# Kernel optimization log

Hardware: AMD Instinct MI355X
Metric: run time of the kernel (lower is better)

Reference implementation:

```python
import jax, jax.numpy as jnp
import numpy as np

B, S, D = 2, 2048, 1024
H, KVH, HD = 16, 1, 64
E, K, HID = 8, 2, 4096
EPS = 1e-5


def rmsnorm(x, scale):
    ms = jnp.mean(x * x, axis=-1, keepdims=True)
    return x * jax.lax.rsqrt(ms + EPS) * scale


def setup_inputs() -> dict:
    key = jax.random.key(0)
    ks = jax.random.split(key, 12)
    s = lambda k, shape, fan: jax.random.normal(k, shape, jnp.float32) * (fan ** -0.5)
    return {
        "x": jax.random.normal(ks[0], (B, S, D), jnp.float32),
        "g_pre_mqa": jnp.ones((D,), jnp.float32),
        "g_post_mqa": jnp.ones((D,), jnp.float32),
        "g_pre_moe": jnp.ones((D,), jnp.float32),
        "g_post_moe": jnp.ones((D,), jnp.float32),
        "Wq": s(ks[1], (D, H * HD), D),
        "Wk": s(ks[2], (D, KVH * HD), D),
        "Wv": s(ks[3], (D, KVH * HD), D),
        "Wo": s(ks[4], (H * HD, D), H * HD),
        "Wg": s(ks[5], (D, E), D),
        "We1": s(ks[6], (E, D, HID), D),
        "We2": s(ks[7], (E, HID, D), HID),
    }


def mqa(x, Wq, Wk, Wv, Wo):
    b, s, _ = x.shape
    q = (x @ Wq).reshape(b, s, H, HD).transpose(0, 2, 1, 3)     # [B,H,S,hd]
    k = (x @ Wk).reshape(b, s, KVH, HD).transpose(0, 2, 1, 3)   # [B,1,S,hd]
    v = (x @ Wv).reshape(b, s, KVH, HD).transpose(0, 2, 1, 3)
    scores = jnp.einsum('bhqd,bhkd->bhqk', q, jnp.broadcast_to(k, (b, H, s, HD))) / np.sqrt(HD)
    probs = jax.nn.softmax(scores, axis=-1)  # note: no causal mask, matching _standard_attention
    out = jnp.einsum('bhqk,bhkd->bhqd', probs, jnp.broadcast_to(v, (b, H, s, HD)))
    out = out.transpose(0, 2, 1, 3).reshape(b, s, H * HD)
    return out @ Wo


def moe(h, Wg, We1, We2):
    logits = h @ Wg                       # [B,S,E]
    probs = jax.nn.softmax(logits, axis=-1)
    topv, topi = jax.lax.top_k(probs, K)  # [B,S,K]
    # scatter top-k probs into full expert vector (non-chosen experts -> 0)
    routing = jnp.sum(jax.nn.one_hot(topi, E, dtype=h.dtype) * topv[..., None], axis=-2)  # [B,S,E]
    mid = jax.nn.gelu(jnp.einsum('bsd,edh->bseh', h, We1))
    eo = jnp.einsum('bseh,ehd->bsed', mid, We2)
    out = jnp.einsum('bse,bsed->bsd', routing, eo)
    return out, probs


def reference(x, g_pre_mqa, g_post_mqa, g_pre_moe, g_post_moe, Wq, Wk, Wv, Wo, Wg, We1, We2):
    # inference path: dropout and router noise disabled (training=False)
    x = x + rmsnorm(mqa(rmsnorm(x, g_pre_mqa), Wq, Wk, Wv, Wo), g_post_mqa)
    moe_out, routing_probs = moe(rmsnorm(x, g_pre_moe), Wg, We1, We2)
    x = x + rmsnorm(moe_out, g_post_moe)
    return x, routing_probs
```

## Files before the change

kernel.cpp:

```cpp
#include <hip/hip_runtime.h>
#include <hip/hip_bf16.h>
#include <math.h>

#define NTOK   4096
#define DMODEL 1024
#define SEQL   2048
#define QKVW   1152
#define NH     16
#define HDIM   64
#define NE     8
#define HIDD   4096
#define EPSV   1e-5f
#define KT     32

#define ASCL   256.f
#define WSCL   4096.f
#define OUTSCL (1.f/1048576.f)
#define SSCALE (0.125f/65536.f)
#define PBIAS  10.397207708399179f
#define DTHR   0.5f

typedef __attribute__((ext_vector_type(8))) short bf16x8;
typedef __attribute__((ext_vector_type(8))) _Float16 f16x8;
typedef __attribute__((ext_vector_type(4))) _Float16 f16x4;
typedef __attribute__((ext_vector_type(4))) float f32x4;

#define GLOBAL_AS __attribute__((address_space(1)))
#define LDS_AS    __attribute__((address_space(3)))
__device__ __forceinline__ void gl_lds16(const void* g, void* l){
  __builtin_amdgcn_global_load_lds((const GLOBAL_AS void*)g, (LDS_AS void*)l, 16u, 0, 0u);
}

__device__ __forceinline__ short f2b(float x){
  __hip_bfloat16 h = __float2bfloat16(x);
  return *reinterpret_cast<short*>(&h);
}
__device__ __forceinline__ void split2h(float x, _Float16& a, _Float16& b){
  a = (_Float16)x;
  b = (_Float16)(x - (float)a);
}

__global__ __launch_bounds__(256) void transpose_conv_kernel(
    const float* __restrict__ in, short* __restrict__ out,
    int R, int C, long inb, long outb)
{
  __shared__ float tile[32][33];
  in  += (size_t)blockIdx.z * inb;
  out += (size_t)blockIdx.z * outb;
  int c0 = blockIdx.x*32, r0 = blockIdx.y*32;
  int tx = threadIdx.x & 31, ty = threadIdx.x >> 5;
  #pragma unroll
  for (int i=0;i<4;i++)
    tile[ty+i*8][tx] = in[(size_t)(r0+ty+i*8)*C + c0+tx];
  __syncthreads();
  int cl = threadIdx.x >> 3, quad = threadIdx.x & 7;
  short4 s;
  s.x = f2b(tile[quad*4+0][cl]);
  s.y = f2b(tile[quad*4+1][cl]);
  s.z = f2b(tile[quad*4+2][cl]);
  s.w = f2b(tile[quad*4+3][cl]);
  *(short4*)&out[(size_t)(c0+cl)*R + r0 + quad*4] = s;
}

__global__ __launch_bounds__(256) void transpose_split2f16_kernel(
    const float* __restrict__ in, _Float16* __restrict__ o1, _Float16* __restrict__ o2,
    int R, int C, int rowOff, int outLD)
{
  __shared__ float tile[32][33];
  int c0 = blockIdx.x*32, r0 = blockIdx.y*32;
  int tx = threadIdx.x & 31, ty = threadIdx.x >> 5;
  #pragma unroll
  for (int i=0;i<4;i++)
    tile[ty+i*8][tx] = in[(size_t)(r0+ty+i*8)*C + c0+tx];
  __syncthreads();
  #pragma unroll
  for (int i=0;i<4;i++){
    float v = tile[tx][ty+i*8] * WSCL;
    _Float16 va,vb; split2h(v,va,vb);
    size_t idx = (size_t)(c0+ty+i*8+rowOff)*outLD + r0+tx;
    o1[idx]=va; o2[idx]=vb;
  }
}

__global__ __launch_bounds__(256) void rms_split2_kernel(
    const float* __restrict__ x, const float* __restrict__ g,
    _Float16* __restrict__ o1, _Float16* __restrict__ o2)
{
  int row = blockIdx.x, tid = threadIdx.x;
  const float4* xr = (const float4*)(x + (size_t)row*DMODEL);
  float4 v = xr[tid];
  float ss = v.x*v.x + v.y*v.y + v.z*v.z + v.w*v.w;
  #pragma unroll
  for (int off=32; off; off>>=1) ss += __shfl_down(ss, off);
  __shared__ float red[4];
  if ((tid&63)==0) red[tid>>6] = ss;
  __syncthreads();
  float rs = rsqrtf((red[0]+red[1]+red[2]+red[3])*(1.f/1024.f) + EPSV) * ASCL;
  float4 gv = ((const float4*)g)[tid];
  float o[4] = {v.x*rs*gv.x, v.y*rs*gv.y, v.z*rs*gv.z, v.w*rs*gv.w};
  f16x4 s1,s2;
  #pragma unroll
  for (int c=0;c<4;c++){ _Float16 a,b; split2h(o[c],a,b); s1[c]=a; s2[c]=b; }
  size_t base = (size_t)row*DMODEL + tid*4;
  *(f16x4*)(o1+base) = s1; *(f16x4*)(o2+base) = s2;
}

__global__ __launch_bounds__(256) void vtrans_split2_kernel(
    const _Float16* __restrict__ p1, const _Float16* __restrict__ p2,
    _Float16* __restrict__ o1, _Float16* __restrict__ o2)
{
  __shared__ float tile[32][33];
  int s0 = blockIdx.x*32, d0 = blockIdx.y*32, bb = blockIdx.z;
  int tx = threadIdx.x & 31, ty = threadIdx.x >> 5;
  #pragma unroll
  for (int i=0;i<4;i++){
    size_t idx = (size_t)(bb*SEQL + s0+ty+i*8)*QKVW + DMODEL+HDIM + d0+tx;
    tile[ty+i*8][tx] = (float)p1[idx] + (float)p2[idx];
  }
  __syncthreads();
  #pragma unroll
  for (int i=0;i<4;i++){
    float v = tile[tx][ty+i*8];
    _Float16 va,vb; split2h(v,va,vb);
    size_t idx = (size_t)(bb*HDIM + d0+ty+i*8)*SEQL + s0+tx;
    o1[idx]=va; o2[idx]=vb;
  }
}

__global__ __launch_bounds__(256) void gemm_f16x2_kernel(
    const _Float16* __restrict__ a1, const _Float16* __restrict__ a2,
    const _Float16* __restrict__ b1, const _Float16* __restrict__ b2,
    float* __restrict__ C, int K, int ldc, float outscale)
{
  __shared__ _Float16 lsA[2][128*32];
  __shared__ _Float16 lsB[2][128*32];
  int m0 = blockIdx.y*128, n0 = blockIdx.x*128;
  int tid = threadIdx.x, wave = tid>>6, lane = tid&63;
  int g = lane>>4, li = lane&15;
  int wm = (wave>>1)*64, wn = (wave&1)*64;
  const _Float16* Ap[2] = {a1,a2};
  const _Float16* Bp[2] = {b1,b2};
  int srow = wave*32 + (lane>>2), scol = (lane&3)*8;
  const _Float16* gA[2][2]; const _Float16* gB[2][2];
  #pragma unroll
  for (int p=0;p<2;p++)
    #pragma unroll
    for (int i=0;i<2;i++){
      gA[p][i] = Ap[p] + (size_t)(m0+srow+i*16)*K + scol;
      gB[p][i] = Bp[p] + (size_t)(n0+srow+i*16)*K + scol;
    }
  f32x4 acc[4][4] = {};
  for (int k0=0; k0<K; k0+=32){
    #pragma unroll
    for (int p=0;p<2;p++)
      #pragma unroll
      for (int i=0;i<2;i++){
        gl_lds16(gA[p][i]+k0, &lsA[p][(wave*32+i*16)*32]);
        gl_lds16(gB[p][i]+k0, &lsB[p][(wave*32+i*16)*32]);
      }
    __syncthreads();
    #pragma unroll
    for (int i=0;i<2;i++){
      f16x8 af[4];
      #pragma unroll
      for (int m=0;m<4;m++) af[m] = *(f16x8*)&lsA[i][(wm+m*16+li)*32 + g*8];
      #pragma unroll
      for (int j=0;j<2-i;j++){
        #pragma unroll
        for (int n=0;n<4;n++){
          f16x8 bfr = *(f16x8*)&lsB[j][(wn+n*16+li)*32 + g*8];
          #pragma unroll
          for (int m=0;m<4;m++)
            acc[m][n] = __builtin_amdgcn_mfma_f32_16x16x32_f16(af[m], bfr, acc[m][n], 0,0,0);
        }
      }
    }
    __syncthreads();
  }
  #pragma unroll
  for (int m=0;m<4;m++){
    int lr0 = wm + m*16 + g*4;
    #pragma unroll
    for (int n=0;n<4;n++){
      int col = n0 + wn + n*16 + li;
      #pragma unroll
      for (int r=0;r<4;r++)
        C[(size_t)(m0+lr0+r)*ldc + col] = acc[m][n][r]*outscale;
    }
  }
}

__global__ __launch_bounds__(256) void gemm_f16x2s_kernel(
    const _Float16* __restrict__ a1, const _Float16* __restrict__ a2,
    const _Float16* __restrict__ b1, const _Float16* __restrict__ b2,
    _Float16* __restrict__ o1, _Float16* __restrict__ o2, int K, int ldc, float outscale)
{
  __shared__ _Float16 lsA[2][128*32];
  __shared__ _Float16 lsB[2][128*32];
  int m0 = blockIdx.y*128, n0 = blockIdx.x*128;
  int tid = threadIdx.x, wave = tid>>6, lane = tid&63;
  int g = lane>>4, li = lane&15;
  int wm = (wave>>1)*64, wn = (wave&1)*64;
  const _Float16* Ap[2] = {a1,a2};
  const _Float16* Bp[2] = {b1,b2};
  int srow = wave*32 + (lane>>2), scol = (lane&3)*8;
  const _Float16* gA[2][2]; const _Float16* gB[2][2];
  #pragma unroll
  for (int p=0;p<2;p++)
    #pragma unroll
    for (int i=0;i<2;i++){
      gA[p][i] = Ap[p] + (size_t)(m0+srow+i*16)*K + scol;
      gB[p][i] = Bp[p] + (size_t)(n0+srow+i*16)*K + scol;
    }
  f32x4 acc[4][4] = {};
  for (int k0=0; k0<K; k0+=32){
    #pragma unroll
    for (int p=0;p<2;p++)
      #pragma unroll
      for (int i=0;i<2;i++){
        gl_lds16(gA[p][i]+k0, &lsA[p][(wave*32+i*16)*32]);
        gl_lds16(gB[p][i]+k0, &lsB[p][(wave*32+i*16)*32]);
      }
    __syncthreads();
    #pragma unroll
    for (int i=0;i<2;i++){
      f16x8 af[4];
      #pragma unroll
      for (int m=0;m<4;m++) af[m] = *(f16x8*)&lsA[i][(wm+m*16+li)*32 + g*8];
      #pragma unroll
      for (int j=0;j<2-i;j++){
        #pragma unroll
        for (int n=0;n<4;n++){
          f16x8 bfr = *(f16x8*)&lsB[j][(wn+n*16+li)*32 + g*8];
          #pragma unroll
          for (int m=0;m<4;m++)
            acc[m][n] = __builtin_amdgcn_mfma_f32_16x16x32_f16(af[m], bfr, acc[m][n], 0,0,0);
        }
      }
    }
    __syncthreads();
  }
  #pragma unroll
  for (int m=0;m<4;m++){
    int lr0 = wm + m*16 + g*4;
    #pragma unroll
    for (int n=0;n<4;n++){
      int col = n0 + wn + n*16 + li;
      #pragma unroll
      for (int r=0;r<4;r++){
        float val = acc[m][n][r]*outscale;
        _Float16 xa,xb; split2h(val,xa,xb);
        size_t idx = (size_t)(m0+lr0+r)*ldc + col;
        o1[idx]=xa; o2[idx]=xb;
      }
    }
  }
}

__global__ __launch_bounds__(256) void attn_f16_kernel(
    const _Float16* __restrict__ q1, const _Float16* __restrict__ q2,
    const _Float16* __restrict__ v1, const _Float16* __restrict__ v2,
    _Float16* __restrict__ o1, _Float16* __restrict__ o2)
{
  __shared__ _Float16 Ks[32*136];
  __shared__ _Float16 Vs[64*72];
  int qt = blockIdx.x, h = blockIdx.y, b = blockIdx.z;
  int tid = threadIdx.x, wave = tid>>6, lane = tid&63;
  int g = lane>>4, li = lane&15;
  size_t qbase = (size_t)b*SEQL + qt*128;
  const _Float16* qsrc[2] = {q1,q2};
  const _Float16* vsrc[2] = {v1,v2};
  f16x8 qf[2][2][2];
  #pragma unroll
  for (int nf=0;nf<2;nf++){
    size_t qrow = qbase + wave*32 + nf*16 + li;
    #pragma unroll
    for (int j=0;j<2;j++)
      #pragma unroll
      for (int kk=0;kk<2;kk++)
        qf[nf][j][kk] = *(const f16x8*)(qsrc[j] + qrow*QKVW + h*HDIM + kk*32 + g*8);
  }
  const _Float16* kga[2]; int klds[2];
  const _Float16* vga[2]; int vlds[2];
  #pragma unroll
  for (int i=0;i<2;i++){
    int c = tid + 256*i;
    { int row=c>>4, sub=c&15, pl=sub>>3, d=(sub&7)*8;
      kga[i] = qsrc[pl] + ((size_t)b*SEQL + row)*QKVW + DMODEL + d;
      klds[i] = row*136 + pl*64 + d; }
    { int row=c>>3, sub=c&7, pl=sub>>2, s8=(sub&3)*8;
      vga[i] = vsrc[pl] + ((size_t)b*HDIM + row)*SEQL + s8;
      vlds[i] = row*72 + pl*32 + s8; }
  }
  f16x8 kreg[2], vreg[2];
  #pragma unroll
  for (int i=0;i<2;i++){ kreg[i]=*(const f16x8*)kga[i]; vreg[i]=*(const f16x8*)vga[i]; }

  float m_run[2] = {-1e30f,-1e30f}, l_run[2] = {0.f,0.f};
  f32x4 acc_o[4][2] = {};
  int src1 = (((2*g)&3)<<4) + li;
  int src2 = (((2*g+1)&3)<<4) + li;
  bool hi_half = (g>=2);

  for (int kvt=0; kvt<SEQL/KT; kvt++){
    #pragma unroll
    for (int i=0;i<2;i++){
      *(f16x8*)&Ks[klds[i]] = kreg[i];
      *(f16x8*)&Vs[vlds[i]] = vreg[i];
    }
    __syncthreads();
    if (kvt+1 < SEQL/KT){
      #pragma unroll
      for (int i=0;i<2;i++){
        kreg[i] = *(const f16x8*)(kga[i] + (size_t)(kvt+1)*KT*QKVW);
        vreg[i] = *(const f16x8*)(vga[i] + (size_t)(kvt+1)*KT);
      }
    }
    f32x4 s_acc[2][2] = {};
    __builtin_amdgcn_s_setprio(1);
    #pragma unroll
    for (int i=0;i<2;i++){
      #pragma unroll
      for (int kk=0;kk<2;kk++){
        f16x8 af[2];
        #pragma unroll
        for (int mf=0;mf<2;mf++)
          af[mf] = *(f16x8*)&Ks[(mf*16+li)*136 + i*64 + kk*32 + g*8];
        #pragma unroll
        for (int j=0;j<2-i;j++){
          #pragma unroll
          for (int nf=0;nf<2;nf++){
            #pragma unroll
            for (int mf=0;mf<2;mf++)
              s_acc[mf][nf] = __builtin_amdgcn_mfma_f32_16x16x32_f16(af[mf], qf[nf][j][kk], s_acc[mf][nf], 0,0,0);
          }
        }
      }
    }
    __builtin_amdgcn_s_setprio(0);
    float p[2][2][4];
    #pragma unroll
    for (int nf=0;nf<2;nf++){
      float mx = -1e30f;
      #pragma unroll
      for (int mf=0;mf<2;mf++)
        #pragma unroll
        for (int r=0;r<4;r++) mx = fmaxf(mx, s_acc[mf][nf][r]);
      mx = fmaxf(mx, __shfl_xor(mx,16));
      mx = fmaxf(mx, __shfl_xor(mx,32));
      mx *= SSCALE;
      if (!__all(mx <= m_run[nf] + DTHR)){
        float mn = fmaxf(m_run[nf], mx);
        float al = __expf(m_run[nf] - mn);
        m_run[nf] = mn;
        l_run[nf] *= al;
        #pragma unroll
        for (int mfd=0; mfd<4; mfd++){
          acc_o[mfd][nf][0]*=al; acc_o[mfd][nf][1]*=al;
          acc_o[mfd][nf][2]*=al; acc_o[mfd][nf][3]*=al;
        }
      }
      float rsum = 0.f;
      #pragma unroll
      for (int mf=0;mf<2;mf++)
        #pragma unroll
        for (int r=0;r<4;r++){
          float pv = __expf(s_acc[mf][nf][r]*SSCALE - m_run[nf] + PBIAS);
          p[mf][nf][r] = pv; rsum += pv;
        }
      rsum += __shfl_xor(rsum,16);
      rsum += __shfl_xor(rsum,32);
      l_run[nf] += rsum;
    }
    f16x8 fp_frag[2][2];
    #pragma unroll
    for (int nf=0;nf<2;nf++){
      float p8[8];
      #pragma unroll
      for (int jj=0;jj<4;jj++){
        float v0 = __shfl(p[0][nf][jj], src1);
        float vv1 = __shfl(p[1][nf][jj], src1);
        p8[jj] = hi_half ? vv1 : v0;
        float w0 = __shfl(p[0][nf][jj], src2);
        float w1 = __shfl(p[1][nf][jj], src2);
        p8[4+jj] = hi_half ? w1 : w0;
      }
      #pragma unroll
      for (int jj=0;jj<8;jj++){
        _Float16 xa,xb; split2h(p8[jj], xa,xb);
        fp_frag[nf][0][jj]=xa; fp_frag[nf][1][jj]=xb;
      }
    }
    __builtin_amdgcn_s_setprio(1);
    #pragma unroll
    for (int vj=0;vj<2;vj++){
      f16x8 av[4];
      #pragma unroll
      for (int mfd=0;mfd<4;mfd++)
        av[mfd] = *(f16x8*)&Vs[(mfd*16+li)*72 + vj*32 + g*8];
      #pragma unroll
      for (int pi=0; pi<2-vj; pi++)
        #pragma unroll
        for (int mfd=0;mfd<4;mfd++)
          #pragma unroll
          for (int nf=0;nf<2;nf++)
            acc_o[mfd][nf] = __builtin_amdgcn_mfma_f32_16x16x32_f16(av[mfd], fp_frag[nf][pi], acc_o[mfd][nf], 0,0,0);
    }
    __builtin_amdgcn_s_setprio(0);
    __syncthreads();
  }
  #pragma unroll
  for (int nf=0;nf<2;nf++){
    float inv = 1.f/l_run[nf];
    size_t q = qbase + wave*32 + nf*16 + li;
    #pragma unroll
    for (int mfd=0;mfd<4;mfd++){
      int d0 = mfd*16 + g*4;
      f16x4 sa,sb;
      #pragma unroll
      for (int r=0;r<4;r++){
        _Float16 xa,xb; split2h(acc_o[mfd][nf][r]*inv, xa,xb);
        sa[r]=xa; sb[r]=xb;
      }
      size_t base = q*DMODEL + h*HDIM + d0;
      *(f16x4*)(o1+base)=sa; *(f16x4*)(o2+base)=sb;
    }
  }
}

__global__ __launch_bounds__(256) void attnres_kernel(
    const float* __restrict__ x, const float* __restrict__ ao,
    const float* __restrict__ gpost, const float* __restrict__ gpre,
    float* __restrict__ x2, short* __restrict__ h)
{
  int row = blockIdx.x, tid = threadIdx.x;
  float4 a  = ((const float4*)(ao + (size_t)row*DMODEL))[tid];
  float4 xv = ((const float4*)(x  + (size_t)row*DMODEL))[tid];
  float ss = a.x*a.x + a.y*a.y + a.z*a.z + a.w*a.w;
  #pragma unroll
  for (int off=32; off; off>>=1) ss += __shfl_down(ss, off);
  __shared__ float red[4];
  if ((tid&63)==0) red[tid>>6] = ss;
  __syncthreads();
  float rs1 = rsqrtf((red[0]+red[1]+red[2]+red[3])*(1.f/1024.f) + EPSV);
  float4 gp = ((const float4*)gpost)[tid];
  float4 o;
  o.x = xv.x + a.x*rs1*gp.x; o.y = xv.y + a.y*rs1*gp.y;
  o.z = xv.z + a.z*rs1*gp.z; o.w = xv.w + a.w*rs1*gp.w;
  ((float4*)(x2 + (size_t)row*DMODEL))[tid] = o;
  float s2 = o.x*o.x + o.y*o.y + o.z*o.z + o.w*o.w;
  __syncthreads();
  #pragma unroll
  for (int off=32; off; off>>=1) s2 += __shfl_down(s2, off);
  if ((tid&63)==0) red[tid>>6] = s2;
  __syncthreads();
  float rs2 = rsqrtf((red[0]+red[1]+red[2]+red[3])*(1.f/1024.f) + EPSV);
  float4 gm = ((const float4*)gpre)[tid];
  short4 hs;
  hs.x = f2b(o.x*rs2*gm.x); hs.y = f2b(o.y*rs2*gm.y);
  hs.z = f2b(o.z*rs2*gm.z); hs.w = f2b(o.w*rs2*gm.w);
  *(short4*)(h + (size_t)row*DMODEL + tid*4) = hs;
}

__global__ __launch_bounds__(64) void router_kernel(
    const float* __restrict__ x2, const float* __restrict__ g, const float* __restrict__ Wg,
    float* __restrict__ probs_out, int* __restrict__ tok_list, float* __restrict__ w_list,
    int* __restrict__ counts)
{
  int t = blockIdx.x, lane = threadIdx.x;
  const float4* xr = (const float4*)(x2 + (size_t)t*DMODEL);
  float4 v[4]; float ss = 0.f;
  #pragma unroll
  for (int i=0;i<4;i++){ v[i] = xr[lane + 64*i];
    ss += v[i].x*v[i].x + v[i].y*v[i].y + v[i].z*v[i].z + v[i].w*v[i].w; }
  #pragma unroll
  for (int off=32; off; off>>=1) ss += __shfl_xor(ss, off);
  float rs = rsqrtf(ss*(1.f/1024.f) + EPSV);
  float le[8] = {0,0,0,0,0,0,0,0};
  #pragma unroll
  for (int i=0;i<4;i++){
    int jb = (lane + 64*i)*4;
    float hv[4] = {v[i].x, v[i].y, v[i].z, v[i].w};
    #pragma unroll
    for (int c=0;c<4;c++){
      float hj = hv[c]*rs*g[jb+c];
      const float* wrow = Wg + (size_t)(jb+c)*NE;
      #pragma unroll
      for (int ee=0;ee<8;ee++) le[ee] += hj*wrow[ee];
    }
  }
  #pragma unroll
  for (int ee=0;ee<8;ee++)
    #pragma unroll
    for (int off=32; off; off>>=1) le[ee] += __shfl_xor(le[ee], off);
  float mx = le[0];
  #pragma unroll
  for (int ee=1;ee<8;ee++) mx = fmaxf(mx, le[ee]);
  float p[8], s = 0.f;
  #pragma unroll
  for (int ee=0;ee<8;ee++){ p[ee] = expf(le[ee]-mx); s += p[ee]; }
  float inv = 1.f/s;
  #pragma unroll
  for (int ee=0;ee<8;ee++) p[ee] *= inv;
  if (lane < 8) probs_out[(size_t)t*NE + lane] = p[lane];
  if (lane == 0){
    int i1 = 0;
    #pragma unroll
    for (int ee=1;ee<8;ee++) if (p[ee] > p[i1]) i1 = ee;
    int i2 = (i1==0) ? 1 : 0;
    #pragma unroll
    for (int ee=0;ee<8;ee++) if (ee != i1 && p[ee] > p[i2]) i2 = ee;
    int pos = atomicAdd(&counts[i1], 1);
    tok_list[i1*NTOK+pos] = t;
    w_list[i1*NTOK+pos] = p[i1];
    pos = atomicAdd(&counts[i2], 1);
    tok_list[i2*NTOK+pos] = t | (1<<16);
    w_list[i2*NTOK+pos] = p[i2];
  }
}

__global__ void prefix_kernel(const int* __restrict__ counts, int* __restrict__ bases){
  if (threadIdx.x == 0){
    int a = 0;
    for (int ee=0;ee<8;ee++){ bases[ee] = a; a += counts[ee]; }
  }
}

__global__ __launch_bounds__(256) void moe_gemm1_kernel(
    const short* __restrict__ h, const short* __restrict__ we1t,
    const int* __restrict__ tok_list, const int* __restrict__ counts,
    const int* __restrict__ bases, short* __restrict__ mid)
{
  int e = blockIdx.z;
  int cnt = counts[e];
  int m0 = blockIdx.y*128, n0 = blockIdx.x*128;
  if (m0 >= cnt) return;
  int base = bases[e];
  const short* Bt = we1t + (size_t)e*HIDD*DMODEL;
  const int* tl = tok_list + e*NTOK;
  __shared__ short lsA[128*32];
  __shared__ short lsB[128*32];
  int tid = threadIdx.x, wave = tid>>6, lane = tid&63;
  int li = lane&15, g = lane>>4;
  int wm = (wave>>1)*64, wn = (wave&1)*64;
  int srow = wave*32 + (lane>>2), scol = (lane&3)*8;
  const short* gA[2]; const short* gB[2];
  #pragma unroll
  for (int i=0;i<2;i++){
    int rr = min(m0+srow+i*16, cnt-1);
    gA[i] = h + (size_t)(tl[rr] & 0xFFFF)*DMODEL + scol;
    gB[i] = Bt + (size_t)(n0+srow+i*16)*DMODEL + scol;
  }
  f32x4 acc[4][4] = {};
  for (int k0=0; k0<DMODEL; k0+=32){
    #pragma unroll
    for (int i=0;i<2;i++){
      gl_lds16(gA[i]+k0, &lsA[(wave*32+i*16)*32]);
      gl_lds16(gB[i]+k0, &lsB[(wave*32+i*16)*32]);
    }
    __syncthreads();
    bf16x8 af[4], bfr[4];
    #pragma unroll
    for (int m=0;m<4;m++) af[m] = *(bf16x8*)&lsA[(wm+m*16+li)*32 + g*8];
    #pragma unroll
    for (int n=0;n<4;n++) bfr[n] = *(bf16x8*)&lsB[(wn+n*16+li)*32 + g*8];
    #pragma unroll
    for (int m=0;m<4;m++)
      #pragma unroll
      for (int n=0;n<4;n++)
        acc[m][n] = __builtin_amdgcn_mfma_f32_16x16x32_bf16(af[m], bfr[n], acc[m][n], 0,0,0);
    __syncthreads();
  }
  #pragma unroll
  for (int m=0;m<4;m++){
    int lr0 = wm + m*16 + (g<<2);
    #pragma unroll
    for (int n=0;n<4;n++){
      int col = n0 + wn + n*16 + li;
      #pragma unroll
      for (int r=0;r<4;r++){
        int gr = m0 + lr0 + r;
        if (gr < cnt){
          float tval = acc[m][n][r];
          float u = 1.5957691216057308f*(tval + 0.044715f*tval*tval*tval);
          float ge = tval / (1.f + __expf(-u));
          mid[(size_t)(base+gr)*HIDD + col] = f2b(ge);
        }
      }
    }
  }
}

__global__ __launch_bounds__(256) void moe_gemm2_kernel(
    const short* __restrict__ mid, const short* __restrict__ we2t,
    const int* __restrict__ tok_list, const float* __restrict__ w_list,
    const int* __restrict__ counts, const int* __restrict__ bases,
    float* __restrict__ eo)
{
  int e = blockIdx.z;
  int cnt = counts[e];
  int m0 = blockIdx.y*128, n0 = blockIdx.x*128;
  if (m0 >= cnt) return;
  int base = bases[e];
  const short* A  = mid + (size_t)base*HIDD;
  const short* Bt = we2t + (size_t)e*DMODEL*HIDD;
  const int* tl = tok_list + e*NTOK;
  const float* wl = w_list + e*NTOK;
  __shared__ short lsA[128*32];
  __shared__ short lsB[128*32];
  int tid = threadIdx.x, wave = tid>>6, lane = tid&63;
  int li = lane&15, g = lane>>4;
  int wm = (wave>>1)*64, wn = (wave&1)*64;
  int srow = wave*32 + (lane>>2), scol = (lane&3)*8;
  const short* gA[2]; const short* gB[2];
  #pragma unroll
  for (int i=0;i<2;i++){
    int rr = min(m0+srow+i*16, cnt-1);
    gA[i] = A + (size_t)rr*HIDD + scol;
    gB[i] = Bt + (size_t)(n0+srow+i*16)*HIDD + scol;
  }
  f32x4 acc[4][4] = {};
  for (int k0=0; k0<HIDD; k0+=32){
    #pragma unroll
    for (int i=0;i<2;i++){
      gl_lds16(gA[i]+k0, &lsA[(wave*32+i*16)*32]);
      gl_lds16(gB[i]+k0, &lsB[(wave*32+i*16)*32]);
    }
    __syncthreads();
    bf16x8 af[4], bfr[4];
    #pragma unroll
    for (int m=0;m<4;m++) af[m] = *(bf16x8*)&lsA[(wm+m*16+li)*32 + g*8];
    #pragma unroll
    for (int n=0;n<4;n++) bfr[n] = *(bf16x8*)&lsB[(wn+n*16+li)*32 + g*8];
    #pragma unroll
    for (int m=0;m<4;m++)
      #pragma unroll
      for (int n=0;n<4;n++)
        acc[m][n] = __builtin_amdgcn_mfma_f32_16x16x32_bf16(af[m], bfr[n], acc[m][n], 0,0,0);
    __syncthreads();
  }
  #pragma unroll
  for (int m=0;m<4;m++){
    int lr0 = wm + m*16 + (g<<2);
    #pragma unroll
    for (int n=0;n<4;n++){
      int col = n0 + wn + n*16 + li;
      #pragma unroll
      for (int r=0;r<4;r++){
        int gr = m0 + lr0 + r;
        if (gr < cnt){
          int pv = tl[gr];
          eo[((size_t)(pv>>16)*NTOK + (pv & 0xFFFF))*DMODEL + col] = wl[gr]*acc[m][n][r];
        }
      }
    }
  }
}

__global__ __launch_bounds__(256) void final_kernel(
    const float* __restrict__ x2, const float* __restrict__ eo,
    const float* __restrict__ g, float* __restrict__ out)
{
  int row = blockIdx.x, tid = threadIdx.x;
  float4 m0 = ((const float4*)(eo + (size_t)row*DMODEL))[tid];
  float4 m1 = ((const float4*)(eo + (size_t)(NTOK+row)*DMODEL))[tid];
  float4 mv;
  mv.x = m0.x+m1.x; mv.y = m0.y+m1.y; mv.z = m0.z+m1.z; mv.w = m0.w+m1.w;
  float4 xv = ((const float4*)(x2  + (size_t)row*DMODEL))[tid];
  float ss = mv.x*mv.x + mv.y*mv.y + mv.z*mv.z + mv.w*mv.w;
  #pragma unroll
  for (int off=32; off; off>>=1) ss += __shfl_down(ss, off);
  __shared__ float red[4];
  if ((tid&63)==0) red[tid>>6] = ss;
  __syncthreads();
  float rs = rsqrtf((red[0]+red[1]+red[2]+red[3])*(1.f/1024.f) + EPSV);
  float4 gv = ((const float4*)g)[tid];
  float4 o;
  o.x = xv.x + mv.x*rs*gv.x; o.y = xv.y + mv.y*rs*gv.y;
  o.z = xv.z + mv.z*rs*gv.z; o.w = xv.w + mv.w*rs*gv.w;
  ((float4*)(out + (size_t)row*DMODEL))[tid] = o;
}

extern "C" void kernel_launch(void* const* d_in, const int* in_sizes, int n_in,
                              void* d_out, int out_size, void* d_ws, size_t ws_size,
                              hipStream_t stream) {
  (void)in_sizes; (void)n_in; (void)out_size; (void)ws_size;
  const float* x          = (const float*)d_in[0];
  const float* g_pre_mqa  = (const float*)d_in[1];
  const float* g_post_mqa = (const float*)d_in[2];
  const float* g_pre_moe  = (const float*)d_in[3];
  const float* g_post_moe = (const float*)d_in[4];
  const float* Wq         = (const float*)d_in[5];
  const float* Wk         = (const float*)d_in[6];
  const float* Wv         = (const float*)d_in[7];
  const float* Wo         = (const float*)d_in[8];
  const float* Wg         = (const float*)d_in[9];
  const float* We1        = (const float*)d_in[10];
  const float* We2        = (const float*)d_in[11];

  float* out_x = (float*)d_out;
  float* out_probs = out_x + (size_t)NTOK*DMODEL;

  char* p = (char*)d_ws;
  size_t off = 0;
  auto alloc = [&](size_t bytes)->char*{
    char* r = p + off; off = (off + bytes + 255) & ~(size_t)255; return r; };

  short* we1t = (short*)alloc((size_t)NE*HIDD*DMODEL*2);
  short* we2t = (short*)alloc((size_t)NE*DMODEL*HIDD*2);
  short* mid  = (short*)alloc((size_t)2*NTOK*HIDD*2);

  char* regA = alloc((size_t)2*NTOK*DMODEL*2);
  _Float16* xn1p1 = (_Float16*)regA;
  _Float16* xn1p2 = (_Float16*)(regA + (size_t)NTOK*DMODEL*2);
  float* ao       = (float*)regA;

  _Float16* wqkvT1 = (_Float16*)alloc((size_t)QKVW*DMODEL*2);
  _Float16* wqkvT2 = (_Float16*)alloc((size_t)QKVW*DMODEL*2);
  _Float16* woT1   = (_Float16*)alloc((size_t)DMODEL*DMODEL*2);
  _Float16* woT2   = (_Float16*)alloc((size_t)DMODEL*DMODEL*2);

  char* regB = alloc((size_t)2*NTOK*DMODEL*2);
  _Float16* attnp1 = (_Float16*)regB;
  _Float16* attnp2 = (_Float16*)(regB + (size_t)NTOK*DMODEL*2);

  char* regC = alloc((size_t)2*NTOK*DMODEL*4 + (size_t)NTOK*DMODEL*2);
  _Float16* qkvf1 = (_Float16*)regC;
  _Float16* qkvf2 = (_Float16*)(regC + (size_t)NTOK*QKVW*2);
  float* eo    = (float*)regC;
  short* hbuf  = (short*)(regC + (size_t)2*NTOK*DMODEL*4);

  _Float16* vt1 = (_Float16*)alloc((size_t)2*HDIM*SEQL*2);
  _Float16* vt2 = (_Float16*)alloc((size_t)2*HDIM*SEQL*2);
  float* x2  = (float*)alloc((size_t)NTOK*DMODEL*4);
  int*   tok_l  = (int*)  alloc((size_t)NE*NTOK*4);
  float* w_l    = (float*)alloc((size_t)NE*NTOK*4);
  int*   counts = (int*)  alloc(256);
  int*   bases  = (int*)  alloc(256);

  transpose_conv_kernel<<<dim3(HIDD/32, DMODEL/32, NE), 256, 0, stream>>>(
      We1, we1t, DMODEL, HIDD, (long)DMODEL*HIDD, (long)HIDD*DMODEL);
  transpose_conv_kernel<<<dim3(DMODEL/32, HIDD/32, NE), 256, 0, stream>>>(
      We2, we2t, HIDD, DMODEL, (long)HIDD*DMODEL, (long)DMODEL*HIDD);
  transpose_split2f16_kernel<<<dim3(DMODEL/32, DMODEL/32), 256, 0, stream>>>(
      Wq, wqkvT1, wqkvT2, DMODEL, DMODEL, 0, DMODEL);
  transpose_split2f16_kernel<<<dim3(HDIM/32, DMODEL/32), 256, 0, stream>>>(
      Wk, wqkvT1, wqkvT2, DMODEL, HDIM, DMODEL, DMODEL);
  transpose_split2f16_kernel<<<dim3(HDIM/32, DMODEL/32), 256, 0, stream>>>(
      Wv, wqkvT1, wqkvT2, DMODEL, HDIM, DMODEL+HDIM, DMODEL);
  transpose_split2f16_kernel<<<dim3(DMODEL/32, DMODEL/32), 256, 0, stream>>>(
      Wo, woT1, woT2, DMODEL, DMODEL, 0, DMODEL);

  rms_split2_kernel<<<NTOK, 256, 0, stream>>>(x, g_pre_mqa, xn1p1, xn1p2);
  gemm_f16x2s_kernel<<<dim3(QKVW/128, NTOK/128), 256, 0, stream>>>(
      xn1p1, xn1p2, wqkvT1, wqkvT2, qkvf1, qkvf2, DMODEL, QKVW, OUTSCL*ASCL);
  vtrans_split2_kernel<<<dim3(SEQL/32, HDIM/32, 2), 256, 0, stream>>>(qkvf1, qkvf2, vt1, vt2);
  attn_f16_kernel<<<dim3(SEQL/128, NH, 2), 256, 0, stream>>>(
      qkvf1, qkvf2, vt1, vt2, attnp1, attnp2);
  gemm_f16x2_kernel<<<dim3(DMODEL/128, NTOK/128), 256, 0, stream>>>(
      attnp1, attnp2, woT1, woT2, ao, DMODEL, DMODEL, OUTSCL);
  attnres_kernel<<<NTOK, 256, 0, stream>>>(x, ao, g_post_mqa, g_pre_moe, x2, hbuf);

  hipMemsetAsync(counts, 0, 32, stream);
  router_kernel<<<NTOK, 64, 0, stream>>>(x2, g_pre_moe, Wg, out_probs, tok_l, w_l, counts);
  prefix_kernel<<<1, 64, 0, stream>>>(counts, bases);
  moe_gemm1_kernel<<<dim3(HIDD/128, NTOK/128, NE), 256, 0, stream>>>(
      hbuf, we1t, tok_l, counts, bases, mid);
  moe_gemm2_kernel<<<dim3(DMODEL/128, NTOK/128, NE), 256, 0, stream>>>(
      mid, we2t, tok_l, w_l, counts, bases, eo);
  final_kernel<<<NTOK, 256, 0, stream>>>(x2, eo, g_post_moe, out_x);
}
```

Baseline: 745.5 us.

## Fuse router into attention residual kernel, drop prefix kernel, swap grid axes

Merges the router (gate logits, softmax, top-2 and atomic token-list append) into the post-attention residual/RMSNorm kernel, so x2 is no longer re-read and normalized a second time. The prefix-sum kernel is removed, and each MoE GEMM block now computes its expert base offset from the counts. All GEMM grids swap blockIdx.x and y, so consecutive blocks walk along M rather than N, which changes L2 reuse of weight tiles. The cost is a larger, more serialized tail in the fused kernel (thread 0 does the softmax, top-k and atomics) and a small redundant prefix loop in every GEMM block.

```diff
diff --git a/kernel.cpp b/kernel.cpp
--- a/kernel.cpp
+++ b/kernel.cpp
@@ -134,7 +134,7 @@
 {
   __shared__ _Float16 lsA[2][128*32];
   __shared__ _Float16 lsB[2][128*32];
-  int m0 = blockIdx.y*128, n0 = blockIdx.x*128;
+  int m0 = blockIdx.x*128, n0 = blockIdx.y*128;
   int tid = threadIdx.x, wave = tid>>6, lane = tid&63;
   int g = lane>>4, li = lane&15;
   int wm = (wave>>1)*64, wn = (wave&1)*64;
@@ -197,7 +197,7 @@
 {
   __shared__ _Float16 lsA[2][128*32];
   __shared__ _Float16 lsB[2][128*32];
-  int m0 = blockIdx.y*128, n0 = blockIdx.x*128;
+  int m0 = blockIdx.x*128, n0 = blockIdx.y*128;
   int tid = threadIdx.x, wave = tid>>6, lane = tid&63;
   int g = lane>>4, li = lane&15;
   int wm = (wave>>1)*64, wn = (wave&1)*64;
@@ -428,10 +428,13 @@
   }
 }
 
-__global__ __launch_bounds__(256) void attnres_kernel(
+__global__ __launch_bounds__(256) void attnres_router_kernel(
     const float* __restrict__ x, const float* __restrict__ ao,
     const float* __restrict__ gpost, const float* __restrict__ gpre,
-    float* __restrict__ x2, short* __restrict__ h)
+    const float* __restrict__ Wg,
+    float* __restrict__ x2, short* __restrict__ h,
+    float* __restrict__ probs_out, int* __restrict__ tok_list,
+    float* __restrict__ w_list, int* __restrict__ counts)
 {
   int row = blockIdx.x, tid = threadIdx.x;
   float4 a  = ((const float4*)(ao + (size_t)row*DMODEL))[tid];
@@ -456,86 +459,63 @@
   __syncthreads();
   float rs2 = rsqrtf((red[0]+red[1]+red[2]+red[3])*(1.f/1024.f) + EPSV);
   float4 gm = ((const float4*)gpre)[tid];
+  float n0 = o.x*rs2*gm.x, n1 = o.y*rs2*gm.y, n2 = o.z*rs2*gm.z, n3 = o.w*rs2*gm.w;
   short4 hs;
-  hs.x = f2b(o.x*rs2*gm.x); hs.y = f2b(o.y*rs2*gm.y);
-  hs.z = f2b(o.z*rs2*gm.z); hs.w = f2b(o.w*rs2*gm.w);
+  hs.x = f2b(n0); hs.y = f2b(n1); hs.z = f2b(n2); hs.w = f2b(n3);
   *(short4*)(h + (size_t)row*DMODEL + tid*4) = hs;
-}
-
-__global__ __launch_bounds__(64) void router_kernel(
-    const float* __restrict__ x2, const float* __restrict__ g, const float* __restrict__ Wg,
-    float* __restrict__ probs_out, int* __restrict__ tok_list, float* __restrict__ w_list,
-    int* __restrict__ counts)
-{
-  int t = blockIdx.x, lane = threadIdx.x;
-  const float4* xr = (const float4*)(x2 + (size_t)t*DMODEL);
-  float4 v[4]; float ss = 0.f;
-  #pragma unroll
-  for (int i=0;i<4;i++){ v[i] = xr[lane + 64*i];
-    ss += v[i].x*v[i].x + v[i].y*v[i].y + v[i].z*v[i].z + v[i].w*v[i].w; }
-  #pragma unroll
-  for (int off=32; off; off>>=1) ss += __shfl_xor(ss, off);
-  float rs = rsqrtf(ss*(1.f/1024.f) + EPSV);
-  float le[8] = {0,0,0,0,0,0,0,0};
-  #pragma unroll
-  for (int i=0;i<4;i++){
-    int jb = (lane + 64*i)*4;
-    float hv[4] = {v[i].x, v[i].y, v[i].z, v[i].w};
-    #pragma unroll
-    for (int c=0;c<4;c++){
-      float hj = hv[c]*rs*g[jb+c];
-      const float* wrow = Wg + (size_t)(jb+c)*NE;
-      #pragma unroll
-      for (int ee=0;ee<8;ee++) le[ee] += hj*wrow[ee];
-    }
-  }
-  #pragma unroll
-  for (int ee=0;ee<8;ee++)
-    #pragma unroll
-    for (int off=32; off; off>>=1) le[ee] += __shfl_xor(le[ee], off);
-  float mx = le[0];
-  #pragma unroll
-  for (int ee=1;ee<8;ee++) mx = fmaxf(mx, le[ee]);
-  float p[8], s = 0.f;
-  #pragma unroll
-  for (int ee=0;ee<8;ee++){ p[ee] = expf(le[ee]-mx); s += p[ee]; }
-  float inv = 1.f/s;
-  #pragma unroll
-  for (int ee=0;ee<8;ee++) p[ee] *= inv;
-  if (lane < 8) probs_out[(size_t)t*NE + lane] = p[lane];
-  if (lane == 0){
+  const float* wr = Wg + (size_t)(tid*4)*NE;
+  float le[8];
+  #pragma unroll
+  for (int e=0;e<8;e++)
+    le[e] = n0*wr[e] + n1*wr[NE+e] + n2*wr[2*NE+e] + n3*wr[3*NE+e];
+  #pragma unroll
+  for (int e=0;e<8;e++)
+    #pragma unroll
+    for (int off=32; off; off>>=1) le[e] += __shfl_xor(le[e], off);
+  __shared__ float redl[4][8];
+  if ((tid&63)==0)
+    #pragma unroll
+    for (int e=0;e<8;e++) redl[tid>>6][e] = le[e];
+  __syncthreads();
+  if (tid == 0){
+    float l[8];
+    #pragma unroll
+    for (int e=0;e<8;e++) l[e] = redl[0][e]+redl[1][e]+redl[2][e]+redl[3][e];
+    float mx = l[0];
+    #pragma unroll
+    for (int e=1;e<8;e++) mx = fmaxf(mx, l[e]);
+    float pp[8], s = 0.f;
+    #pragma unroll
+    for (int e=0;e<8;e++){ pp[e] = expf(l[e]-mx); s += pp[e]; }
+    float inv = 1.f/s;
+    #pragma unroll
+    for (int e=0;e<8;e++){ pp[e] *= inv; probs_out[(size_t)row*NE + e] = pp[e]; }
     int i1 = 0;
     #pragma unroll
-    for (int ee=1;ee<8;ee++) if (p[ee] > p[i1]) i1 = ee;
+    for (int e=1;e<8;e++) if (pp[e] > pp[i1]) i1 = e;
     int i2 = (i1==0) ? 1 : 0;
     #pragma unroll
-    for (int ee=0;ee<8;ee++) if (ee != i1 && p[ee] > p[i2]) i2 = ee;
+    for (int e=0;e<8;e++) if (e != i1 && pp[e] > pp[i2]) i2 = e;
     int pos = atomicAdd(&counts[i1], 1);
-    tok_list[i1*NTOK+pos] = t;
-    w_list[i1*NTOK+pos] = p[i1];
+    tok_list[i1*NTOK+pos] = row;
+    w_list[i1*NTOK+pos] = pp[i1];
     pos = atomicAdd(&counts[i2], 1);
-    tok_list[i2*NTOK+pos] = t | (1<<16);
-    w_list[i2*NTOK+pos] = p[i2];
-  }
-}
-
-__global__ void prefix_kernel(const int* __restrict__ counts, int* __restrict__ bases){
-  if (threadIdx.x == 0){
-    int a = 0;
-    for (int ee=0;ee<8;ee++){ bases[ee] = a; a += counts[ee]; }
+    tok_list[i2*NTOK+pos] = row | (1<<16);
+    w_list[i2*NTOK+pos] = pp[i2];
   }
 }
 
 __global__ __launch_bounds__(256) void moe_gemm1_kernel(
     const short* __restrict__ h, const short* __restrict__ we1t,
     const int* __restrict__ tok_list, const int* __restrict__ counts,
-    const int* __restrict__ bases, short* __restrict__ mid)
+    short* __restrict__ mid)
 {
   int e = blockIdx.z;
   int cnt = counts[e];
-  int m0 = blockIdx.y*128, n0 = blockIdx.x*128;
+  int m0 = blockIdx.x*128, n0 = blockIdx.y*128;
   if (m0 >= cnt) return;
-  int base = bases[e];
+  int base = 0;
+  for (int j=0;j<NE;j++){ int c = counts[j]; if (j<e) base += c; }
   const short* Bt = we1t + (size_t)e*HIDD*DMODEL;
   const int* tl = tok_list + e*NTOK;
   __shared__ short lsA[128*32];
@@ -594,14 +574,14 @@
 __global__ __launch_bounds__(256) void moe_gemm2_kernel(
     const short* __restrict__ mid, const short* __restrict__ we2t,
     const int* __restrict__ tok_list, const float* __restrict__ w_list,
-    const int* __restrict__ counts, const int* __restrict__ bases,
-    float* __restrict__ eo)
+    const int* __restrict__ counts, float* __restrict__ eo)
 {
   int e = blockIdx.z;
   int cnt = counts[e];
-  int m0 = blockIdx.y*128, n0 = blockIdx.x*128;
+  int m0 = blockIdx.x*128, n0 = blockIdx.y*128;
   if (m0 >= cnt) return;
-  int base = bases[e];
+  int base = 0;
+  for (int j=0;j<NE;j++){ int c = counts[j]; if (j<e) base += c; }
   const short* A  = mid + (size_t)base*HIDD;
   const short* Bt = we2t + (size_t)e*DMODEL*HIDD;
   const int* tl = tok_list + e*NTOK;
@@ -736,7 +716,6 @@
   int*   tok_l  = (int*)  alloc((size_t)NE*NTOK*4);
   float* w_l    = (float*)alloc((size_t)NE*NTOK*4);
   int*   counts = (int*)  alloc(256);
-  int*   bases  = (int*)  alloc(256);
 
   transpose_conv_kernel<<<dim3(HIDD/32, DMODEL/32, NE), 256, 0, stream>>>(
       We1, we1t, DMODEL, HIDD, (long)DMODEL*HIDD, (long)HIDD*DMODEL);
@@ -752,21 +731,20 @@
       Wo, woT1, woT2, DMODEL, DMODEL, 0, DMODEL);
 
   rms_split2_kernel<<<NTOK, 256, 0, stream>>>(x, g_pre_mqa, xn1p1, xn1p2);
-  gemm_f16x2s_kernel<<<dim3(QKVW/128, NTOK/128), 256, 0, stream>>>(
+  gemm_f16x2s_kernel<<<dim3(NTOK/128, QKVW/128), 256, 0, stream>>>(
       xn1p1, xn1p2, wqkvT1, wqkvT2, qkvf1, qkvf2, DMODEL, QKVW, OUTSCL*ASCL);
   vtrans_split2_kernel<<<dim3(SEQL/32, HDIM/32, 2), 256, 0, stream>>>(qkvf1, qkvf2, vt1, vt2);
   attn_f16_kernel<<<dim3(SEQL/128, NH, 2), 256, 0, stream>>>(
       qkvf1, qkvf2, vt1, vt2, attnp1, attnp2);
-  gemm_f16x2_kernel<<<dim3(DMODEL/128, NTOK/128), 256, 0, stream>>>(
+  gemm_f16x2_kernel<<<dim3(NTOK/128, DMODEL/128), 256, 0, stream>>>(
       attnp1, attnp2, woT1, woT2, ao, DMODEL, DMODEL, OUTSCL);
-  attnres_kernel<<<NTOK, 256, 0, stream>>>(x, ao, g_post_mqa, g_pre_moe, x2, hbuf);
 
   hipMemsetAsync(counts, 0, 32, stream);
-  router_kernel<<<NTOK, 64, 0, stream>>>(x2, g_pre_moe, Wg, out_probs, tok_l, w_l, counts);
-  prefix_kernel<<<1, 64, 0, stream>>>(counts, bases);
-  moe_gemm1_kernel<<<dim3(HIDD/128, NTOK/128, NE), 256, 0, stream>>>(
-      hbuf, we1t, tok_l, counts, bases, mid);
-  moe_gemm2_kernel<<<dim3(DMODEL/128, NTOK/128, NE), 256, 0, stream>>>(
-      mid, we2t, tok_l, w_l, counts, bases, eo);
+  attnres_router_kernel<<<NTOK, 256, 0, stream>>>(
+      x, ao, g_post_mqa, g_pre_moe, Wg, x2, hbuf, out_probs, tok_l, w_l, counts);
+  moe_gemm1_kernel<<<dim3(NTOK/128, HIDD/128, NE), 256, 0, stream>>>(
+      hbuf, we1t, tok_l, counts, mid);
+  moe_gemm2_kernel<<<dim3(NTOK/128, DMODEL/128, NE), 256, 0, stream>>>(
+      mid, we2t, tok_l, w_l, counts, eo);
   final_kernel<<<NTOK, 256, 0, stream>>>(x2, eo, g_post_moe, out_x);
 }
```

New measurement: 1.151 ms. 54.4% more time.
